# Performance work log

Measured on AMD Instinct MI355X. Metric: run time of the kernel, lower is better.

Reference implementation:

```python
import jax, jax.numpy as jnp
import numpy as np

DIM = 768
HEADS = 12
HEAD_DIM = DIM // HEADS  # 64
GRID = 48               # H = W = 48 tokens
RANK = 8                # LoRA rank


def setup_inputs() -> dict:
    key = jax.random.key(0)
    ks = jax.random.split(key, 20)
    s = 0.02
    inp = {
        "x": jax.random.normal(ks[0], (1, GRID, GRID, DIM), dtype=jnp.float32),
        "Wq": jax.random.normal(ks[1], (DIM, DIM), dtype=jnp.float32) * s,
        "bq": jax.random.normal(ks[2], (DIM,), dtype=jnp.float32) * s,
        "Wk": jax.random.normal(ks[3], (DIM, DIM), dtype=jnp.float32) * s,
        "bk": jax.random.normal(ks[4], (DIM,), dtype=jnp.float32) * s,
        "Wv": jax.random.normal(ks[5], (DIM, DIM), dtype=jnp.float32) * s,
        "bv": jax.random.normal(ks[6], (DIM,), dtype=jnp.float32) * s,
        "Wp": jax.random.normal(ks[7], (DIM, DIM), dtype=jnp.float32) * s,
        "bp": jax.random.normal(ks[8], (DIM,), dtype=jnp.float32) * s,
        "rel_pos_h": jax.random.normal(ks[9], (2 * GRID - 1, HEAD_DIM), dtype=jnp.float32) * s,
        "rel_pos_w": jax.random.normal(ks[10], (2 * GRID - 1, HEAD_DIM), dtype=jnp.float32) * s,
        "Aq": jax.random.normal(ks[11], (DIM, RANK), dtype=jnp.float32) * s,
        "Bq": jax.random.normal(ks[12], (RANK, DIM), dtype=jnp.float32) * s,
        "Ak": jax.random.normal(ks[13], (DIM, RANK), dtype=jnp.float32) * s,
        "Bk": jax.random.normal(ks[14], (RANK, DIM), dtype=jnp.float32) * s,
        "Av": jax.random.normal(ks[15], (DIM, RANK), dtype=jnp.float32) * s,
        "Bv": jax.random.normal(ks[16], (RANK, DIM), dtype=jnp.float32) * s,
    }
    return inp


def _get_rel_pos(size, rel_pos):
    # q_size == k_size == size, rel_pos has exactly 2*size-1 rows -> direct lookup
    idx = jnp.arange(size)[:, None] - jnp.arange(size)[None, :] + (size - 1)
    return rel_pos[idx]  # (size, size, head_dim)


def reference(x, Wq, bq, Wk, bk, Wv, bv, Wp, bp, rel_pos_h, rel_pos_w,
              Aq, Bq, Ak, Bk, Av, Bv):
    B, H, W, _ = x.shape
    N = H * W
    scale = HEAD_DIM ** -0.5

    # QKV projections + LoRA additions
    q = x @ Wq + bq + (x @ Aq) @ Bq
    k = x @ Wk + bk + (x @ Ak) @ Bk
    v = x @ Wv + bv + (x @ Av) @ Bv

    # (B, heads, N, head_dim)
    q = q.reshape(B, N, HEADS, HEAD_DIM).transpose(0, 2, 1, 3)
    k = k.reshape(B, N, HEADS, HEAD_DIM).transpose(0, 2, 1, 3)
    v = v.reshape(B, N, HEADS, HEAD_DIM).transpose(0, 2, 1, 3)

    attn = jnp.einsum('bhnc,bhmc->bhnm', q, k) * scale  # (B, heads, N, N)

    # Decomposed relative position bias (SAM add_decomposed_rel_pos)
    Rh = _get_rel_pos(H, rel_pos_h)  # (H, H, c)
    Rw = _get_rel_pos(W, rel_pos_w)  # (W, W, c)
    r_q = q.reshape(B, HEADS, H, W, HEAD_DIM)
    rel_h = jnp.einsum('bnhwc,hkc->bnhwk', r_q, Rh)  # (B, heads, H, W, H)
    rel_w = jnp.einsum('bnhwc,wkc->bnhwk', r_q, Rw)  # (B, heads, H, W, W)
    attn = (attn.reshape(B, HEADS, H, W, H, W)
            + rel_h[..., :, None] + rel_w[..., None, :]).reshape(B, HEADS, N, N)

    attn = jax.nn.softmax(attn, axis=-1)
    out = jnp.einsum('bhnm,bhmc->bhnc', attn, v)        # (B, heads, N, c)
    out = out.transpose(0, 2, 1, 3).reshape(B, H, W, DIM)
    return out @ Wp + bp
```

## Files before the change

kernel.cpp:

```cpp
#include <hip/hip_runtime.h>


#define DIM   768
#define HEADS 12
#define HD    64
#define NTOK  2304
#define RANK  8
#define GRD   48
#define CHUNKS 4
#define KTILES 9
#define LOG2E 1.44269504088896f

typedef __attribute__((ext_vector_type(8))) short bf16x8;
typedef __attribute__((ext_vector_type(4))) float f32x4;
typedef unsigned short ushort_t;

__device__ __forceinline__ unsigned short f2bf(float x) {
    union { float f; unsigned u; } v; v.f = x;
    unsigned r = v.u + 0x7fffu + ((v.u >> 16) & 1u);
    return (unsigned short)(r >> 16);
}

__global__ __launch_bounds__(256) void k_convert_x(
    const float* __restrict__ x, ushort_t* __restrict__ xb,
    const float* __restrict__ rph, const float* __restrict__ rpw,
    ushort_t* __restrict__ rphb, ushort_t* __restrict__ rpwb) {
    if (blockIdx.x < 1728) {
        int idx = (blockIdx.x * 256 + threadIdx.x) * 4;
        float4 v = *(const float4*)(x + idx);
        ushort4 o = make_ushort4(f2bf(v.x), f2bf(v.y), f2bf(v.z), f2bf(v.w));
        *(ushort4*)(xb + idx) = o;
    } else {
        int e = ((blockIdx.x - 1728) * 256 + threadIdx.x) * 4;
        const int TSZ = (2 * GRD - 1) * HD;
        if (e < TSZ) {
            float4 v = *(const float4*)(rph + e);
            ushort4 o = make_ushort4(f2bf(v.x), f2bf(v.y), f2bf(v.z), f2bf(v.w));
            *(ushort4*)(rphb + e) = o;
        } else if (e < 2 * TSZ) {
            float4 v = *(const float4*)(rpw + e - TSZ);
            ushort4 o = make_ushort4(f2bf(v.x), f2bf(v.y), f2bf(v.z), f2bf(v.w));
            *(ushort4*)(rpwb + e - TSZ) = o;
        }
    }
}

__global__ __launch_bounds__(256) void k_fold(
    const float* __restrict__ Wq, const float* __restrict__ Wk,
    const float* __restrict__ Wv, const float* __restrict__ Wp,
    const float* __restrict__ Aq, const float* __restrict__ Bq,
    const float* __restrict__ Ak, const float* __restrict__ Bk,
    const float* __restrict__ Av, const float* __restrict__ Bv,
    ushort_t* __restrict__ WT) {
    int kb = blockIdx.x * 32;
    int nb = blockIdx.y * 32;
    int qkv = nb / DIM;
    int nmod = nb % DIM;
    const float* W = (qkv == 0) ? Wq : (qkv == 1) ? Wk : (qkv == 2) ? Wv : Wp;
    const float* A = (qkv == 0) ? Aq : (qkv == 1) ? Ak : Av;
    const float* B = (qkv == 0) ? Bq : (qkv == 1) ? Bk : Bv;

    __shared__ float T[32][33];
    for (int i = threadIdx.x; i < 1024; i += 256) {
        int kl = i / 32, nl = i % 32;
        float v = W[(kb + kl) * DIM + nmod + nl];
        if (qkv < 3) {
            #pragma unroll
            for (int r = 0; r < RANK; r++)
                v += A[(kb + kl) * RANK + r] * B[r * DIM + nmod + nl];
        }
        T[kl][nl] = v;
    }
    __syncthreads();
    for (int i = threadIdx.x; i < 1024; i += 256) {
        int nl = i / 32, kl = i % 32;
        WT[(size_t)(nb + nl) * DIM + kb + kl] = f2bf(T[kl][nl]);
    }
}

__global__ __launch_bounds__(256) void k_gemm_qkv(
    const ushort_t* __restrict__ xb, const ushort_t* __restrict__ WT,
    const float* __restrict__ bq, const float* __restrict__ bk,
    const float* __restrict__ bv,
    ushort_t* __restrict__ Qb, ushort_t* __restrict__ Kb,
    ushort_t* __restrict__ Vtb) {
    __shared__ __align__(16) ushort_t As[128 * 40];
    __shared__ __align__(16) ushort_t Bs[128 * 40];
    int tid = threadIdx.x;
    int wave = tid >> 6, lane = tid & 63, quad = lane >> 4, l16 = lane & 15;
    int wx = wave & 1, wy = wave >> 1;
    int nb = blockIdx.x * 128, mb = blockIdx.y * 128;

    f32x4 zero = {0.f, 0.f, 0.f, 0.f};
    f32x4 acc[4][4];
    #pragma unroll
    for (int i = 0; i < 4; i++)
        #pragma unroll
        for (int j = 0; j < 4; j++) acc[i][j] = zero;

    const ushort_t* Ag = xb + (size_t)(mb + (tid >> 1)) * DIM + (tid & 1) * 16;
    const ushort_t* Bg = WT + (size_t)(nb + (tid >> 1)) * DIM + (tid & 1) * 16;
    int sidx = (tid >> 1) * 40 + (tid & 1) * 16;

    for (int k0 = 0; k0 < DIM; k0 += 32) {
        uint4 a0 = *(const uint4*)(Ag + k0);
        uint4 a1 = *(const uint4*)(Ag + k0 + 8);
        uint4 b0 = *(const uint4*)(Bg + k0);
        uint4 b1 = *(const uint4*)(Bg + k0 + 8);
        __syncthreads();
        *(uint4*)&As[sidx] = a0;  *(uint4*)&As[sidx + 8] = a1;
        *(uint4*)&Bs[sidx] = b0;  *(uint4*)&Bs[sidx + 8] = b1;
        __syncthreads();
        bf16x8 af[4], bf[4];
        #pragma unroll
        for (int i = 0; i < 4; i++)
            af[i] = *(const bf16x8*)&As[(wy * 64 + i * 16 + l16) * 40 + quad * 8];
        #pragma unroll
        for (int j = 0; j < 4; j++)
            bf[j] = *(const bf16x8*)&Bs[(wx * 64 + j * 16 + l16) * 40 + quad * 8];
        #pragma unroll
        for (int i = 0; i < 4; i++)
            #pragma unroll
            for (int j = 0; j < 4; j++)
                acc[i][j] = __builtin_amdgcn_mfma_f32_16x16x32_bf16(af[i], bf[j], acc[i][j], 0, 0, 0);
    }

    #pragma unroll
    for (int j = 0; j < 4; j++) {
        int col = nb + wx * 64 + j * 16 + l16;
        int qkv = col / DIM, rem = col % DIM;
        int hh = rem >> 6, cc = rem & 63;
        const float* bias = (qkv == 0) ? bq : (qkv == 1) ? bk : bv;
        float bval = bias[rem];
        #pragma unroll
        for (int i = 0; i < 4; i++) {
            #pragma unroll
            for (int r = 0; r < 4; r++) {
                int row = mb + wy * 64 + i * 16 + quad * 4 + r;
                unsigned short o = f2bf(acc[i][j][r] + bval);
                if (qkv == 0)      Qb[(size_t)(hh * NTOK + row) * HD + cc] = o;
                else if (qkv == 1) Kb[(size_t)(hh * NTOK + row) * HD + cc] = o;
                else               Vtb[(size_t)(hh * HD + cc) * NTOK + row] = o;
            }
        }
    }
}

__global__ __launch_bounds__(256) void k_relmm(
    const ushort_t* __restrict__ Qb, const ushort_t* __restrict__ rphb,
    const ushort_t* __restrict__ rpwb, float* __restrict__ relH,
    float* __restrict__ relW) {
    int id = blockIdx.x * 4 + (threadIdx.x >> 6);
    int lane = threadIdx.x & 63, quad = lane >> 4, l16 = lane & 15;
    bool isW = id >= 576;
    int t = isW ? id - 576 : id;
    int h = t / GRD, g = t % GRD;
    const ushort_t* tab = isW ? rpwb : rphb;
    float* outp = isW ? relW : relH;

    f32x4 zero = {0.f, 0.f, 0.f, 0.f};
    f32x4 acc[3][3];
    #pragma unroll
    for (int i = 0; i < 3; i++)
        #pragma unroll
        for (int j = 0; j < 3; j++) acc[i][j] = zero;

    bf16x8 bfr[3][2];
    #pragma unroll
    for (int ct = 0; ct < 3; ct++) {
        int trow = g + 47 - (ct * 16 + l16);
        bfr[ct][0] = *(const bf16x8*)&tab[(size_t)trow * HD + quad * 8];
        bfr[ct][1] = *(const bf16x8*)&tab[(size_t)trow * HD + 32 + quad * 8];
    }
    #pragma unroll
    for (int ms = 0; ms < 3; ms++) {
        int m = ms * 16 + l16;
        int n = isW ? m * GRD + g : g * GRD + m;
        bf16x8 a0 = *(const bf16x8*)&Qb[(size_t)(h * NTOK + n) * HD + quad * 8];
        bf16x8 a1 = *(const bf16x8*)&Qb[(size_t)(h * NTOK + n) * HD + 32 + quad * 8];
        #pragma unroll
        for (int ct = 0; ct < 3; ct++) {
            acc[ms][ct] = __builtin_amdgcn_mfma_f32_16x16x32_bf16(a0, bfr[ct][0], acc[ms][ct], 0, 0, 0);
            acc[ms][ct] = __builtin_amdgcn_mfma_f32_16x16x32_bf16(a1, bfr[ct][1], acc[ms][ct], 0, 0, 0);
        }
    }
    #pragma unroll
    for (int ms = 0; ms < 3; ms++) {
        #pragma unroll
        for (int ct = 0; ct < 3; ct++) {
            #pragma unroll
            for (int r = 0; r < 4; r++) {
                int m = ms * 16 + quad * 4 + r;
                int n = isW ? m * GRD + g : g * GRD + m;
                int col = ct * 16 + l16;
                outp[(size_t)(h * NTOK + n) * GRD + col] = acc[ms][ct][r] * LOG2E;
            }
        }
    }
}

__global__ __launch_bounds__(256) void k_attn(
    const ushort_t* __restrict__ Qb, const ushort_t* __restrict__ Kb,
    const ushort_t* __restrict__ Vtb, const float* __restrict__ relH,
    const float* __restrict__ relW, float* __restrict__ Opart,
    float* __restrict__ Lpart) {
    int qt = blockIdx.x, h = blockIdx.y, chunk = blockIdx.z;
    int tid = threadIdx.x;
    int wave = tid >> 6, lane = tid & 63, quad = lane >> 4, l16 = lane & 15;
    int qbase = qt * 128;
    int kbase = chunk * (KTILES * 64);

    __shared__ __align__(16) ushort_t Ks[64 * 72];
    __shared__ __align__(16) ushort_t Vs[64 * 72];
    __shared__ __align__(16) ushort_t Ps[4][32 * 72];
    __shared__ float rhs[128 * 13];

    bf16x8 qf[2][2];
    #pragma unroll
    for (int s = 0; s < 2; s++) {
        int qrow = qbase + wave * 32 + s * 16 + l16;
        qf[s][0] = *(const bf16x8*)&Qb[(size_t)(h * NTOK + qrow) * HD + quad * 8];
        qf[s][1] = *(const bf16x8*)&Qb[(size_t)(h * NTOK + qrow) * HD + 32 + quad * 8];
    }

    float rwreg[2][4][3];
    #pragma unroll
    for (int s = 0; s < 2; s++)
        #pragma unroll
        for (int r = 0; r < 4; r++) {
            int row = qbase + wave * 32 + s * 16 + quad * 4 + r;
            #pragma unroll
            for (int j = 0; j < 3; j++)
                rwreg[s][r][j] = relW[(size_t)(h * NTOK + row) * GRD + j * 16 + l16];
        }

    for (int i = tid; i < 128 * 12; i += 256) {
        int r = i / 12, c = i % 12;
        rhs[r * 13 + c] = relH[(size_t)(h * NTOK + qbase + r) * GRD + chunk * 12 + c];
    }

    float l_st[2][4] = {{0.f,0.f,0.f,0.f},{0.f,0.f,0.f,0.f}};
    f32x4 zero = {0.f, 0.f, 0.f, 0.f};
    f32x4 oacc[2][4];
    #pragma unroll
    for (int s = 0; s < 2; s++)
        #pragma unroll
        for (int j = 0; j < 4; j++) oacc[s][j] = zero;

    const float scale2 = 0.125f * LOG2E;
    int stg_r = tid >> 2, stg_c = (tid & 3) * 16;
    const ushort_t* Kg = Kb + (size_t)(h * NTOK + stg_r) * HD + stg_c;
    const ushort_t* Vg = Vtb + (size_t)(h * HD + stg_r) * NTOK + stg_c;

    uint4 rk0, rk1, rv0, rv1;
    {
        int kb = kbase;
        rk0 = *(const uint4*)(Kg + (size_t)kb * HD);
        rk1 = *(const uint4*)(Kg + (size_t)kb * HD + 8);
        rv0 = *(const uint4*)(Vg + kb);
        rv1 = *(const uint4*)(Vg + kb + 8);
    }

    for (int kt = 0; kt < KTILES; kt++) {
        __syncthreads();
        *(uint4*)&Ks[stg_r * 72 + stg_c]     = rk0;
        *(uint4*)&Ks[stg_r * 72 + stg_c + 8] = rk1;
        *(uint4*)&Vs[stg_r * 72 + stg_c]     = rv0;
        *(uint4*)&Vs[stg_r * 72 + stg_c + 8] = rv1;
        __syncthreads();

        {
            int ktn = (kt + 1 < KTILES) ? kt + 1 : kt;
            int kb = kbase + ktn * 64;
            rk0 = *(const uint4*)(Kg + (size_t)kb * HD);
            rk1 = *(const uint4*)(Kg + (size_t)kb * HD + 8);
            rv0 = *(const uint4*)(Vg + kb);
            rv1 = *(const uint4*)(Vg + kb + 8);
        }

        f32x4 sv[2][4];
        #pragma unroll
        for (int ct = 0; ct < 4; ct++) {
            bf16x8 kf0 = *(const bf16x8*)&Ks[(ct * 16 + l16) * 72 + quad * 8];
            bf16x8 kf1 = *(const bf16x8*)&Ks[(ct * 16 + l16) * 72 + 32 + quad * 8];
            #pragma unroll
            for (int s = 0; s < 2; s++) {
                f32x4 z = zero;
                z = __builtin_amdgcn_mfma_f32_16x16x32_bf16(qf[s][0], kf0, z, 0, 0, 0);
                z = __builtin_amdgcn_mfma_f32_16x16x32_bf16(qf[s][1], kf1, z, 0, 0, 0);
                sv[s][ct] = z;
            }
        }

        #pragma unroll
        for (int ct = 0; ct < 4; ct++) {
            int m = 4 * kt + ct;
            int khl = m / 3;
            int j = m % 3;
            #pragma unroll
            for (int s = 0; s < 2; s++) {
                #pragma unroll
                for (int r = 0; r < 4; r++) {
                    int rloc = wave * 32 + s * 16 + quad * 4 + r;
                    float v = sv[s][ct][r] * scale2 + rhs[rloc * 13 + khl] + rwreg[s][r][j];
                    float p = __builtin_amdgcn_exp2f(v);
                    l_st[s][r] += p;
                    Ps[wave][(s * 16 + quad * 4 + r) * 72 + ct * 16 + l16] = f2bf(p);
                }
            }
        }

        bf16x8 pf[2][2];
        #pragma unroll
        for (int s = 0; s < 2; s++) {
            pf[s][0] = *(const bf16x8*)&Ps[wave][(s * 16 + l16) * 72 + quad * 8];
            pf[s][1] = *(const bf16x8*)&Ps[wave][(s * 16 + l16) * 72 + 32 + quad * 8];
        }
        #pragma unroll
        for (int ct = 0; ct < 4; ct++) {
            bf16x8 vf0 = *(const bf16x8*)&Vs[(ct * 16 + l16) * 72 + quad * 8];
            bf16x8 vf1 = *(const bf16x8*)&Vs[(ct * 16 + l16) * 72 + 32 + quad * 8];
            #pragma unroll
            for (int s = 0; s < 2; s++) {
                oacc[s][ct] = __builtin_amdgcn_mfma_f32_16x16x32_bf16(pf[s][0], vf0, oacc[s][ct], 0, 0, 0);
                oacc[s][ct] = __builtin_amdgcn_mfma_f32_16x16x32_bf16(pf[s][1], vf1, oacc[s][ct], 0, 0, 0);
            }
        }
    }

    #pragma unroll
    for (int s = 0; s < 2; s++)
        #pragma unroll
        for (int r = 0; r < 4; r++) {
            float l = l_st[s][r];
            l += __shfl_xor(l, 1);
            l += __shfl_xor(l, 2);
            l += __shfl_xor(l, 4);
            l += __shfl_xor(l, 8);
            l_st[s][r] = l;
        }

    size_t obase = (size_t)(chunk * HEADS + h) * NTOK;
    #pragma unroll
    for (int s = 0; s < 2; s++) {
        #pragma unroll
        for (int ct = 0; ct < 4; ct++) {
            #pragma unroll
            for (int r = 0; r < 4; r++) {
                int row = qbase + wave * 32 + s * 16 + quad * 4 + r;
                Opart[(obase + row) * HD + ct * 16 + l16] = oacc[s][ct][r];
            }
        }
        if (l16 == 0) {
            #pragma unroll
            for (int r = 0; r < 4; r++) {
                int row = qbase + wave * 32 + s * 16 + quad * 4 + r;
                Lpart[obase + row] = l_st[s][r];
            }
        }
    }
}

__global__ __launch_bounds__(256) void k_merge(const float* __restrict__ Opart,
                                               const float* __restrict__ Lpart,
                                               ushort_t* __restrict__ Ob) {
    int t = blockIdx.x * 256 + threadIdx.x;
    int e = t * 4;
    int c = e & (HD - 1);
    int row = (e >> 6) % NTOK;
    int h = e / (NTOK * HD);
    const int ostride = HEADS * NTOK * HD;
    float4 s = {0.f, 0.f, 0.f, 0.f};
    float l = 0.f;
    #pragma unroll
    for (int ch = 0; ch < CHUNKS; ch++) {
        float4 v = *(const float4*)&Opart[(size_t)ch * ostride + e];
        s.x += v.x; s.y += v.y; s.z += v.z; s.w += v.w;
        l += Lpart[(size_t)(ch * HEADS + h) * NTOK + row];
    }
    float inv = 1.0f / l;
    ushort4 o = make_ushort4(f2bf(s.x * inv), f2bf(s.y * inv),
                             f2bf(s.z * inv), f2bf(s.w * inv));
    *(ushort4*)&Ob[(size_t)row * DIM + h * HD + c] = o;
}

__global__ __launch_bounds__(256) void k_gemm_proj(
    const ushort_t* __restrict__ Ob, const ushort_t* __restrict__ WTp,
    const float* __restrict__ bp, float* __restrict__ out) {
    __shared__ __align__(16) ushort_t As[128 * 40];
    __shared__ __align__(16) ushort_t Bs[128 * 40];
    int tid = threadIdx.x;
    int wave = tid >> 6, lane = tid & 63, quad = lane >> 4, l16 = lane & 15;
    int wx = wave & 1, wy = wave >> 1;
    int nb = blockIdx.x * 128, mb = blockIdx.y * 128;

    f32x4 zero = {0.f, 0.f, 0.f, 0.f};
    f32x4 acc[4][4];
    #pragma unroll
    for (int i = 0; i < 4; i++)
        #pragma unroll
        for (int j = 0; j < 4; j++) acc[i][j] = zero;

    const ushort_t* Ag = Ob + (size_t)(mb + (tid >> 1)) * DIM + (tid & 1) * 16;
    const ushort_t* Bg = WTp + (size_t)(nb + (tid >> 1)) * DIM + (tid & 1) * 16;
    int sidx = (tid >> 1) * 40 + (tid & 1) * 16;

    for (int k0 = 0; k0 < DIM; k0 += 32) {
        uint4 a0 = *(const uint4*)(Ag + k0);
        uint4 a1 = *(const uint4*)(Ag + k0 + 8);
        uint4 b0 = *(const uint4*)(Bg + k0);
        uint4 b1 = *(const uint4*)(Bg + k0 + 8);
        __syncthreads();
        *(uint4*)&As[sidx] = a0;  *(uint4*)&As[sidx + 8] = a1;
        *(uint4*)&Bs[sidx] = b0;  *(uint4*)&Bs[sidx + 8] = b1;
        __syncthreads();
        bf16x8 af[4], bf[4];
        #pragma unroll
        for (int i = 0; i < 4; i++)
            af[i] = *(const bf16x8*)&As[(wy * 64 + i * 16 + l16) * 40 + quad * 8];
        #pragma unroll
        for (int j = 0; j < 4; j++)
            bf[j] = *(const bf16x8*)&Bs[(wx * 64 + j * 16 + l16) * 40 + quad * 8];
        #pragma unroll
        for (int i = 0; i < 4; i++)
            #pragma unroll
            for (int j = 0; j < 4; j++)
                acc[i][j] = __builtin_amdgcn_mfma_f32_16x16x32_bf16(af[i], bf[j], acc[i][j], 0, 0, 0);
    }

    #pragma unroll
    for (int j = 0; j < 4; j++) {
        int col = nb + wx * 64 + j * 16 + l16;
        float bval = bp[col];
        #pragma unroll
        for (int i = 0; i < 4; i++) {
            #pragma unroll
            for (int r = 0; r < 4; r++) {
                int row = mb + wy * 64 + i * 16 + quad * 4 + r;
                out[(size_t)row * DIM + col] = acc[i][j][r] + bval;
            }
        }
    }
}

extern "C" void kernel_launch(void* const* d_in, const int* in_sizes, int n_in,
                              void* d_out, int out_size, void* d_ws, size_t ws_size,
                              hipStream_t stream) {
    const float* x   = (const float*)d_in[0];
    const float* Wq  = (const float*)d_in[1];
    const float* bq  = (const float*)d_in[2];
    const float* Wk  = (const float*)d_in[3];
    const float* bk  = (const float*)d_in[4];
    const float* Wv  = (const float*)d_in[5];
    const float* bv  = (const float*)d_in[6];
    const float* Wp  = (const float*)d_in[7];
    const float* bp  = (const float*)d_in[8];
    const float* rph = (const float*)d_in[9];
    const float* rpw = (const float*)d_in[10];
    const float* Aq  = (const float*)d_in[11];
    const float* Bq  = (const float*)d_in[12];
    const float* Ak  = (const float*)d_in[13];
    const float* Bk  = (const float*)d_in[14];
    const float* Av  = (const float*)d_in[15];
    const float* Bv  = (const float*)d_in[16];
    float* out = (float*)d_out;

    char* w = (char*)d_ws;
    size_t off = 0;
    auto carve = [&](size_t bytes) {
        char* p = w + off;
        off += (bytes + 255) & ~(size_t)255;
        return p;
    };
    ushort_t* xb    = (ushort_t*)carve((size_t)NTOK * DIM * 2);
    ushort_t* WT    = (ushort_t*)carve((size_t)4 * DIM * DIM * 2);
    ushort_t* Qb    = (ushort_t*)carve((size_t)HEADS * NTOK * HD * 2);
    ushort_t* Kb    = (ushort_t*)carve((size_t)HEADS * NTOK * HD * 2);
    ushort_t* Vtb   = (ushort_t*)carve((size_t)HEADS * HD * NTOK * 2);
    float*    relH  = (float*)carve((size_t)HEADS * NTOK * GRD * 4);
    float*    relW  = (float*)carve((size_t)HEADS * NTOK * GRD * 4);
    ushort_t* Ob    = (ushort_t*)carve((size_t)NTOK * DIM * 2);
    float*    Opart = (float*)carve((size_t)CHUNKS * HEADS * NTOK * HD * 4);
    float*    Lpart = (float*)carve((size_t)CHUNKS * HEADS * NTOK * 4);
    ushort_t* rphb  = (ushort_t*)carve((size_t)(2 * GRD - 1) * HD * 2);
    ushort_t* rpwb  = (ushort_t*)carve((size_t)(2 * GRD - 1) * HD * 2);

    k_convert_x<<<dim3(1728 + 12), dim3(256), 0, stream>>>(x, xb, rph, rpw, rphb, rpwb);
    k_fold<<<dim3(DIM / 32, 4 * DIM / 32), dim3(256), 0, stream>>>(
        Wq, Wk, Wv, Wp, Aq, Bq, Ak, Bk, Av, Bv, WT);
    k_gemm_qkv<<<dim3(18, 18), dim3(256), 0, stream>>>(
        xb, WT, bq, bk, bv, Qb, Kb, Vtb);
    k_relmm<<<dim3(288), dim3(256), 0, stream>>>(
        Qb, rphb, rpwb, relH, relW);
    k_attn<<<dim3(NTOK / 128, HEADS, CHUNKS), dim3(256), 0, stream>>>(
        Qb, Kb, Vtb, relH, relW, Opart, Lpart);
    k_merge<<<dim3(HEADS * NTOK * HD / (256 * 4)), dim3(256), 0, stream>>>(
        Opart, Lpart, Ob);
    k_gemm_proj<<<dim3(6, 18), dim3(256), 0, stream>>>(
        Ob, WT + (size_t)3 * DIM * DIM, bp, out);
}
```

Before: 216.0 us.

## Split attention keys across waves, direct-to-LDS loads in QKV GEMM

The attention kernel now uses 64-query tiles, with each wave owning a slice of keys instead of a slice of queries. K and V fragments are loaded straight from global memory into registers, and the per-wave partial outputs are reduced through LDS. Opart is written in a transposed layout, and the merge kernel transposes it back through shared memory. The QKV GEMM switches to global_load_lds direct-to-LDS copies with an unpadded tile, which may add LDS bank conflicts. The relW bias is stored as bf16, which loses some precision.

```diff
diff --git a/kernel.cpp b/kernel.cpp
--- a/kernel.cpp
+++ b/kernel.cpp
@@ -8,7 +8,6 @@
 #define RANK  8
 #define GRD   48
 #define CHUNKS 4
-#define KTILES 9
 #define LOG2E 1.44269504088896f
 
 typedef __attribute__((ext_vector_type(8))) short bf16x8;
@@ -19,6 +18,12 @@
     union { float f; unsigned u; } v; v.f = x;
     unsigned r = v.u + 0x7fffu + ((v.u >> 16) & 1u);
     return (unsigned short)(r >> 16);
+}
+
+__device__ __forceinline__ void gload_lds16(const ushort_t* g, ushort_t* l) {
+    __builtin_amdgcn_global_load_lds(
+        (const __attribute__((address_space(1))) unsigned int*)g,
+        (__attribute__((address_space(3))) unsigned int*)l, 16, 0, 0);
 }
 
 __global__ __launch_bounds__(256) void k_convert_x(
@@ -84,8 +89,8 @@
     const float* __restrict__ bv,
     ushort_t* __restrict__ Qb, ushort_t* __restrict__ Kb,
     ushort_t* __restrict__ Vtb) {
-    __shared__ __align__(16) ushort_t As[128 * 40];
-    __shared__ __align__(16) ushort_t Bs[128 * 40];
+    __shared__ __align__(16) ushort_t As[128 * 32];
+    __shared__ __align__(16) ushort_t Bs[128 * 32];
     int tid = threadIdx.x;
     int wave = tid >> 6, lane = tid & 63, quad = lane >> 4, l16 = lane & 15;
     int wx = wave & 1, wy = wave >> 1;
@@ -98,26 +103,27 @@
         #pragma unroll
         for (int j = 0; j < 4; j++) acc[i][j] = zero;
 
-    const ushort_t* Ag = xb + (size_t)(mb + (tid >> 1)) * DIM + (tid & 1) * 16;
-    const ushort_t* Bg = WT + (size_t)(nb + (tid >> 1)) * DIM + (tid & 1) * 16;
-    int sidx = (tid >> 1) * 40 + (tid & 1) * 16;
+    int rl = lane >> 2;
+    int cl = (lane & 3) * 8;
+    const ushort_t* gA = xb + (size_t)(mb + wave * 32 + rl) * DIM + cl;
+    const ushort_t* gB = WT + (size_t)(nb + wave * 32 + rl) * DIM + cl;
+    ushort_t* lA = &As[(wave * 32) * 32];
+    ushort_t* lB = &Bs[(wave * 32) * 32];
 
     for (int k0 = 0; k0 < DIM; k0 += 32) {
-        uint4 a0 = *(const uint4*)(Ag + k0);
-        uint4 a1 = *(const uint4*)(Ag + k0 + 8);
-        uint4 b0 = *(const uint4*)(Bg + k0);
-        uint4 b1 = *(const uint4*)(Bg + k0 + 8);
         __syncthreads();
-        *(uint4*)&As[sidx] = a0;  *(uint4*)&As[sidx + 8] = a1;
-        *(uint4*)&Bs[sidx] = b0;  *(uint4*)&Bs[sidx + 8] = b1;
+        gload_lds16(gA + k0,            lA);
+        gload_lds16(gA + k0 + 16 * DIM, lA + 16 * 32);
+        gload_lds16(gB + k0,            lB);
+        gload_lds16(gB + k0 + 16 * DIM, lB + 16 * 32);
         __syncthreads();
         bf16x8 af[4], bf[4];
         #pragma unroll
         for (int i = 0; i < 4; i++)
-            af[i] = *(const bf16x8*)&As[(wy * 64 + i * 16 + l16) * 40 + quad * 8];
+            af[i] = *(const bf16x8*)&As[(wy * 64 + i * 16 + l16) * 32 + quad * 8];
         #pragma unroll
         for (int j = 0; j < 4; j++)
-            bf[j] = *(const bf16x8*)&Bs[(wx * 64 + j * 16 + l16) * 40 + quad * 8];
+            bf[j] = *(const bf16x8*)&Bs[(wx * 64 + j * 16 + l16) * 32 + quad * 8];
         #pragma unroll
         for (int i = 0; i < 4; i++)
             #pragma unroll
@@ -199,7 +205,7 @@
     }
 }
 
-__global__ __launch_bounds__(256) void k_attn(
+__global__ __launch_bounds__(256, 2) void k_attn(
     const ushort_t* __restrict__ Qb, const ushort_t* __restrict__ Kb,
     const ushort_t* __restrict__ Vtb, const float* __restrict__ relH,
     const float* __restrict__ relW, float* __restrict__ Opart,
@@ -207,181 +213,199 @@
     int qt = blockIdx.x, h = blockIdx.y, chunk = blockIdx.z;
     int tid = threadIdx.x;
     int wave = tid >> 6, lane = tid & 63, quad = lane >> 4, l16 = lane & 15;
-    int qbase = qt * 128;
-    int kbase = chunk * (KTILES * 64);
-
-    __shared__ __align__(16) ushort_t Ks[64 * 72];
-    __shared__ __align__(16) ushort_t Vs[64 * 72];
-    __shared__ __align__(16) ushort_t Ps[4][32 * 72];
-    __shared__ float rhs[128 * 13];
-
-    bf16x8 qf[2][2];
-    #pragma unroll
-    for (int s = 0; s < 2; s++) {
-        int qrow = qbase + wave * 32 + s * 16 + l16;
-        qf[s][0] = *(const bf16x8*)&Qb[(size_t)(h * NTOK + qrow) * HD + quad * 8];
-        qf[s][1] = *(const bf16x8*)&Qb[(size_t)(h * NTOK + qrow) * HD + 32 + quad * 8];
-    }
-
-    float rwreg[2][4][3];
-    #pragma unroll
-    for (int s = 0; s < 2; s++)
-        #pragma unroll
-        for (int r = 0; r < 4; r++) {
-            int row = qbase + wave * 32 + s * 16 + quad * 4 + r;
-            #pragma unroll
-            for (int j = 0; j < 3; j++)
-                rwreg[s][r][j] = relW[(size_t)(h * NTOK + row) * GRD + j * 16 + l16];
-        }
-
-    for (int i = tid; i < 128 * 12; i += 256) {
+    int qbase = qt * 64;
+    int kbase = chunk * 576;
+
+    __shared__ __align__(16) ushort_t Ps[4][64 * 40];
+    __shared__ __align__(16) ushort_t rws[64 * 52];
+    __shared__ float rhs[64 * 13];
+    __shared__ float Lred[4][64];
+
+    for (int i = tid; i < 64 * 48; i += 256) {
+        int r = i / 48, c = i % 48;
+        rws[r * 52 + c] = f2bf(relW[(size_t)(h * NTOK + qbase + r) * GRD + c]);
+    }
+    for (int i = tid; i < 64 * 12; i += 256) {
         int r = i / 12, c = i % 12;
         rhs[r * 13 + c] = relH[(size_t)(h * NTOK + qbase + r) * GRD + chunk * 12 + c];
     }
 
-    float l_st[2][4] = {{0.f,0.f,0.f,0.f},{0.f,0.f,0.f,0.f}};
+    bf16x8 qf[4][2];
+    #pragma unroll
+    for (int qs = 0; qs < 4; qs++) {
+        int qrow = qbase + qs * 16 + l16;
+        qf[qs][0] = *(const bf16x8*)&Qb[(size_t)(h * NTOK + qrow) * HD + quad * 8];
+        qf[qs][1] = *(const bf16x8*)&Qb[(size_t)(h * NTOK + qrow) * HD + 32 + quad * 8];
+    }
+
+    float lacc[4] = {0.f, 0.f, 0.f, 0.f};
     f32x4 zero = {0.f, 0.f, 0.f, 0.f};
-    f32x4 oacc[2][4];
-    #pragma unroll
-    for (int s = 0; s < 2; s++)
-        #pragma unroll
-        for (int j = 0; j < 4; j++) oacc[s][j] = zero;
+    f32x4 oacc[4][4];
+    #pragma unroll
+    for (int qs = 0; qs < 4; qs++)
+        #pragma unroll
+        for (int cs = 0; cs < 4; cs++) oacc[qs][cs] = zero;
 
     const float scale2 = 0.125f * LOG2E;
-    int stg_r = tid >> 2, stg_c = (tid & 3) * 16;
-    const ushort_t* Kg = Kb + (size_t)(h * NTOK + stg_r) * HD + stg_c;
-    const ushort_t* Vg = Vtb + (size_t)(h * HD + stg_r) * NTOK + stg_c;
-
-    uint4 rk0, rk1, rv0, rv1;
-    {
-        int kb = kbase;
-        rk0 = *(const uint4*)(Kg + (size_t)kb * HD);
-        rk1 = *(const uint4*)(Kg + (size_t)kb * HD + 8);
-        rv0 = *(const uint4*)(Vg + kb);
-        rv1 = *(const uint4*)(Vg + kb + 8);
-    }
-
-    for (int kt = 0; kt < KTILES; kt++) {
-        __syncthreads();
-        *(uint4*)&Ks[stg_r * 72 + stg_c]     = rk0;
-        *(uint4*)&Ks[stg_r * 72 + stg_c + 8] = rk1;
-        *(uint4*)&Vs[stg_r * 72 + stg_c]     = rv0;
-        *(uint4*)&Vs[stg_r * 72 + stg_c + 8] = rv1;
-        __syncthreads();
-
-        {
-            int ktn = (kt + 1 < KTILES) ? kt + 1 : kt;
-            int kb = kbase + ktn * 64;
-            rk0 = *(const uint4*)(Kg + (size_t)kb * HD);
-            rk1 = *(const uint4*)(Kg + (size_t)kb * HD + 8);
-            rv0 = *(const uint4*)(Vg + kb);
-            rv1 = *(const uint4*)(Vg + kb + 8);
-        }
-
-        f32x4 sv[2][4];
-        #pragma unroll
-        for (int ct = 0; ct < 4; ct++) {
-            bf16x8 kf0 = *(const bf16x8*)&Ks[(ct * 16 + l16) * 72 + quad * 8];
-            bf16x8 kf1 = *(const bf16x8*)&Ks[(ct * 16 + l16) * 72 + 32 + quad * 8];
-            #pragma unroll
-            for (int s = 0; s < 2; s++) {
+    __syncthreads();
+
+    for (int it = 0; it < 5; ++it) {
+        bool full = (it < 4);
+        int keyw = kbase + it * 128 + wave * (full ? 32 : 16);
+
+        bf16x8 kf0a = *(const bf16x8*)&Kb[(size_t)(h * NTOK + keyw + l16) * HD + quad * 8];
+        bf16x8 kf0b = *(const bf16x8*)&Kb[(size_t)(h * NTOK + keyw + l16) * HD + 32 + quad * 8];
+        bf16x8 kf1a, kf1b;
+        if (full) {
+            kf1a = *(const bf16x8*)&Kb[(size_t)(h * NTOK + keyw + 16 + l16) * HD + quad * 8];
+            kf1b = *(const bf16x8*)&Kb[(size_t)(h * NTOK + keyw + 16 + l16) * HD + 32 + quad * 8];
+        }
+        bf16x8 vf[4];
+        #pragma unroll
+        for (int cs = 0; cs < 4; cs++)
+            vf[cs] = *(const bf16x8*)&Vtb[(size_t)(h * HD + cs * 16 + l16) * NTOK + keyw + quad * 8];
+
+        f32x4 st[2][4];
+        #pragma unroll
+        for (int qs = 0; qs < 4; qs++) {
+            f32x4 z = zero;
+            z = __builtin_amdgcn_mfma_f32_16x16x32_bf16(kf0a, qf[qs][0], z, 0, 0, 0);
+            z = __builtin_amdgcn_mfma_f32_16x16x32_bf16(kf0b, qf[qs][1], z, 0, 0, 0);
+            st[0][qs] = z;
+        }
+        if (full) {
+            #pragma unroll
+            for (int qs = 0; qs < 4; qs++) {
                 f32x4 z = zero;
-                z = __builtin_amdgcn_mfma_f32_16x16x32_bf16(qf[s][0], kf0, z, 0, 0, 0);
-                z = __builtin_amdgcn_mfma_f32_16x16x32_bf16(qf[s][1], kf1, z, 0, 0, 0);
-                sv[s][ct] = z;
+                z = __builtin_amdgcn_mfma_f32_16x16x32_bf16(kf1a, qf[qs][0], z, 0, 0, 0);
+                z = __builtin_amdgcn_mfma_f32_16x16x32_bf16(kf1b, qf[qs][1], z, 0, 0, 0);
+                st[1][qs] = z;
             }
         }
 
-        #pragma unroll
-        for (int ct = 0; ct < 4; ct++) {
-            int m = 4 * kt + ct;
-            int khl = m / 3;
-            int j = m % 3;
-            #pragma unroll
-            for (int s = 0; s < 2; s++) {
+        int nks = full ? 2 : 1;
+        for (int ks = 0; ks < nks; ++ks) {
+            int kb4 = keyw + ks * 16 + quad * 4;
+            int kh = kb4 / 48;
+            int khl = kh - chunk * 12;
+            int kw0 = kb4 - kh * 48;
+            #pragma unroll
+            for (int qs = 0; qs < 4; qs++) {
+                int row = qs * 16 + l16;
+                float rh = rhs[row * 13 + khl];
+                uint2 rwp = *(const uint2*)&rws[row * 52 + kw0];
+                float rw0 = __uint_as_float(rwp.x << 16);
+                float rw1 = __uint_as_float(rwp.x & 0xffff0000u);
+                float rw2 = __uint_as_float(rwp.y << 16);
+                float rw3 = __uint_as_float(rwp.y & 0xffff0000u);
+                float p0 = __builtin_amdgcn_exp2f(st[ks][qs][0] * scale2 + rh + rw0);
+                float p1 = __builtin_amdgcn_exp2f(st[ks][qs][1] * scale2 + rh + rw1);
+                float p2 = __builtin_amdgcn_exp2f(st[ks][qs][2] * scale2 + rh + rw2);
+                float p3 = __builtin_amdgcn_exp2f(st[ks][qs][3] * scale2 + rh + rw3);
+                lacc[qs] += (p0 + p1) + (p2 + p3);
+                uint2 w;
+                w.x = (unsigned)f2bf(p0) | ((unsigned)f2bf(p1) << 16);
+                w.y = (unsigned)f2bf(p2) | ((unsigned)f2bf(p3) << 16);
+                *(uint2*)&Ps[wave][row * 40 + ks * 16 + quad * 4] = w;
+            }
+        }
+        if (!full) {
+            uint2 zz; zz.x = 0u; zz.y = 0u;
+            #pragma unroll
+            for (int qs = 0; qs < 4; qs++)
+                *(uint2*)&Ps[wave][(qs * 16 + l16) * 40 + 16 + quad * 4] = zz;
+        }
+
+        #pragma unroll
+        for (int qs = 0; qs < 4; qs++) {
+            bf16x8 pa = *(const bf16x8*)&Ps[wave][(qs * 16 + l16) * 40 + quad * 8];
+            #pragma unroll
+            for (int cs = 0; cs < 4; cs++)
+                oacc[qs][cs] = __builtin_amdgcn_mfma_f32_16x16x32_bf16(pa, vf[cs], oacc[qs][cs], 0, 0, 0);
+        }
+    }
+
+    #pragma unroll
+    for (int qs = 0; qs < 4; qs++) {
+        float l = lacc[qs];
+        l += __shfl_xor(l, 16);
+        l += __shfl_xor(l, 32);
+        lacc[qs] = l;
+    }
+    if (quad == 0) {
+        #pragma unroll
+        for (int qs = 0; qs < 4; qs++) Lred[wave][qs * 16 + l16] = lacc[qs];
+    }
+
+    float* Ored = (float*)&Ps[0][0];
+    __syncthreads();
+    for (int w = 0; w < 4; ++w) {
+        if (wave == w) {
+            #pragma unroll
+            for (int qs = 0; qs < 4; qs++) {
                 #pragma unroll
-                for (int r = 0; r < 4; r++) {
-                    int rloc = wave * 32 + s * 16 + quad * 4 + r;
-                    float v = sv[s][ct][r] * scale2 + rhs[rloc * 13 + khl] + rwreg[s][r][j];
-                    float p = __builtin_amdgcn_exp2f(v);
-                    l_st[s][r] += p;
-                    Ps[wave][(s * 16 + quad * 4 + r) * 72 + ct * 16 + l16] = f2bf(p);
+                for (int cs = 0; cs < 4; cs++) {
+                    int a = (cs * 16 + l16) * 68 + qs * 16 + quad * 4;
+                    if (w == 0) {
+                        *(f32x4*)&Ored[a] = oacc[qs][cs];
+                    } else {
+                        f32x4 t = *(const f32x4*)&Ored[a];
+                        t += oacc[qs][cs];
+                        *(f32x4*)&Ored[a] = t;
+                    }
                 }
             }
         }
-
-        bf16x8 pf[2][2];
-        #pragma unroll
-        for (int s = 0; s < 2; s++) {
-            pf[s][0] = *(const bf16x8*)&Ps[wave][(s * 16 + l16) * 72 + quad * 8];
-            pf[s][1] = *(const bf16x8*)&Ps[wave][(s * 16 + l16) * 72 + 32 + quad * 8];
-        }
-        #pragma unroll
-        for (int ct = 0; ct < 4; ct++) {
-            bf16x8 vf0 = *(const bf16x8*)&Vs[(ct * 16 + l16) * 72 + quad * 8];
-            bf16x8 vf1 = *(const bf16x8*)&Vs[(ct * 16 + l16) * 72 + 32 + quad * 8];
-            #pragma unroll
-            for (int s = 0; s < 2; s++) {
-                oacc[s][ct] = __builtin_amdgcn_mfma_f32_16x16x32_bf16(pf[s][0], vf0, oacc[s][ct], 0, 0, 0);
-                oacc[s][ct] = __builtin_amdgcn_mfma_f32_16x16x32_bf16(pf[s][1], vf1, oacc[s][ct], 0, 0, 0);
-            }
-        }
-    }
-
-    #pragma unroll
-    for (int s = 0; s < 2; s++)
-        #pragma unroll
-        for (int r = 0; r < 4; r++) {
-            float l = l_st[s][r];
-            l += __shfl_xor(l, 1);
-            l += __shfl_xor(l, 2);
-            l += __shfl_xor(l, 4);
-            l += __shfl_xor(l, 8);
-            l_st[s][r] = l;
-        }
-
-    size_t obase = (size_t)(chunk * HEADS + h) * NTOK;
-    #pragma unroll
-    for (int s = 0; s < 2; s++) {
-        #pragma unroll
-        for (int ct = 0; ct < 4; ct++) {
-            #pragma unroll
-            for (int r = 0; r < 4; r++) {
-                int row = qbase + wave * 32 + s * 16 + quad * 4 + r;
-                Opart[(obase + row) * HD + ct * 16 + l16] = oacc[s][ct][r];
-            }
-        }
-        if (l16 == 0) {
-            #pragma unroll
-            for (int r = 0; r < 4; r++) {
-                int row = qbase + wave * 32 + s * 16 + quad * 4 + r;
-                Lpart[obase + row] = l_st[s][r];
-            }
-        }
+        __syncthreads();
+    }
+
+    size_t obase = (size_t)(chunk * HEADS + h) * HD * NTOK;
+    #pragma unroll
+    for (int i = 0; i < 4; i++) {
+        int idx = tid + i * 256;
+        int c = idx >> 4, part = idx & 15;
+        uint4 val = *(const uint4*)&Ored[c * 68 + part * 4];
+        *(uint4*)&Opart[obase + (size_t)c * NTOK + qbase + part * 4] = val;
+    }
+    if (tid < 64) {
+        float s = Lred[0][tid] + Lred[1][tid] + Lred[2][tid] + Lred[3][tid];
+        Lpart[(size_t)(chunk * HEADS + h) * NTOK + qbase + tid] = s;
     }
 }
 
 __global__ __launch_bounds__(256) void k_merge(const float* __restrict__ Opart,
                                                const float* __restrict__ Lpart,
                                                ushort_t* __restrict__ Ob) {
-    int t = blockIdx.x * 256 + threadIdx.x;
-    int e = t * 4;
-    int c = e & (HD - 1);
-    int row = (e >> 6) % NTOK;
-    int h = e / (NTOK * HD);
-    const int ostride = HEADS * NTOK * HD;
-    float4 s = {0.f, 0.f, 0.f, 0.f};
+    int h = blockIdx.x / 36, tb = blockIdx.x % 36;
+    int tok0 = tb * 64;
+    int t = threadIdx.x;
+    int tok = t & 63, cbase = t >> 6;
+
+    float acc[16];
+    #pragma unroll
+    for (int i = 0; i < 16; i++) acc[i] = 0.f;
     float l = 0.f;
-    #pragma unroll
     for (int ch = 0; ch < CHUNKS; ch++) {
-        float4 v = *(const float4*)&Opart[(size_t)ch * ostride + e];
-        s.x += v.x; s.y += v.y; s.z += v.z; s.w += v.w;
-        l += Lpart[(size_t)(ch * HEADS + h) * NTOK + row];
+        size_t base = (size_t)(ch * HEADS + h) * HD * NTOK;
+        #pragma unroll
+        for (int i = 0; i < 16; i++)
+            acc[i] += Opart[base + (size_t)(cbase + i * 4) * NTOK + tok0 + tok];
+        l += Lpart[(size_t)(ch * HEADS + h) * NTOK + tok0 + tok];
     }
     float inv = 1.0f / l;
-    ushort4 o = make_ushort4(f2bf(s.x * inv), f2bf(s.y * inv),
-                             f2bf(s.z * inv), f2bf(s.w * inv));
-    *(ushort4*)&Ob[(size_t)row * DIM + h * HD + c] = o;
+
+    __shared__ ushort_t Tb[64][72];
+    #pragma unroll
+    for (int i = 0; i < 16; i++)
+        Tb[tok][cbase + i * 4] = f2bf(acc[i] * inv);
+    __syncthreads();
+    #pragma unroll
+    for (int i = 0; i < 2; i++) {
+        int idx = t + i * 256;
+        int r = idx >> 3, part = idx & 7;
+        uint4 val = *(const uint4*)&Tb[r][part * 8];
+        *(uint4*)&Ob[(size_t)(tok0 + r) * DIM + h * HD + part * 8] = val;
+    }
 }
 
 __global__ __launch_bounds__(256) void k_gemm_proj(
@@ -492,9 +516,9 @@
         xb, WT, bq, bk, bv, Qb, Kb, Vtb);
     k_relmm<<<dim3(288), dim3(256), 0, stream>>>(
         Qb, rphb, rpwb, relH, relW);
-    k_attn<<<dim3(NTOK / 128, HEADS, CHUNKS), dim3(256), 0, stream>>>(
+    k_attn<<<dim3(NTOK / 64, HEADS, CHUNKS), dim3(256), 0, stream>>>(
         Qb, Kb, Vtb, relH, relW, Opart, Lpart);
-    k_merge<<<dim3(HEADS * NTOK * HD / (256 * 4)), dim3(256), 0, stream>>>(
+    k_merge<<<dim3(HEADS * 36), dim3(256), 0, stream>>>(
         Opart, Lpart, Ob);
     k_gemm_proj<<<dim3(6, 18), dim3(256), 0, stream>>>(
         Ob, WT + (size_t)3 * DIM * DIM, bp, out);
```

After: 234.6 us. +8.6%, slower.
